# Kernel optimization log

Hardware: AMD Instinct MI355X
Metric: run time of the kernel (lower is better)

## Reference

```python
import jax, jax.numpy as jnp
import numpy as np
from jax import lax

T, N, E, F, H, L, HL = 16, 10000, 320000, 128, 256, 64, 256


def setup_inputs() -> dict:
    key = jax.random.key(0)
    ks = iter(jax.random.split(key, 40))
    def nrm(shape, fan_in):
        return jax.random.normal(next(ks), shape, jnp.float32) * (1.0 / np.sqrt(fan_in))
    inp = {}
    inp["xs"] = jax.random.normal(next(ks), (T, N, F), jnp.float32)
    inp["edge_attr"] = jax.random.uniform(next(ks), (E,), jnp.float32)
    # encoder: GCN(F->H), GCN(H->H), Linear(H->L)
    inp["We0"], inp["be0"] = nrm((F, H), F), nrm((H,), H)
    inp["We1"], inp["be1"] = nrm((H, H), H), nrm((H,), H)
    inp["Wfce"], inp["bfce"] = nrm((H, L), H), nrm((L,), L)
    # 2-layer LSTM (torch gate order i,f,g,o; weights stored [in,4H])
    inp["Wih0"], inp["Whh0"] = nrm((L, 4 * HL), HL), nrm((HL, 4 * HL), HL)
    inp["bih0"], inp["bhh0"] = nrm((4 * HL,), HL), nrm((4 * HL,), HL)
    inp["Wih1"], inp["Whh1"] = nrm((HL, 4 * HL), HL), nrm((HL, 4 * HL), HL)
    inp["bih1"], inp["bhh1"] = nrm((4 * HL,), HL), nrm((4 * HL,), HL)
    inp["Whead"], inp["bhead"] = nrm((HL, L), HL), nrm((L,), L)
    # decoder: Linear(L -> N*L), GCN(L->H), GCN(H->H), GCN(H->F)
    inp["Wfcd"], inp["bfcd"] = nrm((L, N * L), L), nrm((N * L,), L)
    inp["Wd0"], inp["bd0"] = nrm((L, H), L), nrm((H,), H)
    inp["Wd1"], inp["bd1"] = nrm((H, H), H), nrm((H,), H)
    inp["Wd2"], inp["bd2"] = nrm((H, F), H), nrm((F,), F)
    inp["edge_index"] = jax.random.randint(next(ks), (2, E), 0, N, jnp.int64)
    return inp


def _forward(xs, edge_attr, We0, be0, We1, be1, Wfce, bfce,
             Wih0, Whh0, bih0, bhh0, Wih1, Whh1, bih1, bhh1,
             Whead, bhead, Wfcd, bfcd, Wd0, bd0, Wd1, bd1, Wd2, bd2,
             edge_index):
    n = xs.shape[1]
    loops = jnp.arange(n)
    src = jnp.concatenate([edge_index[0], loops])  # [E+N] with self-loops
    dst = jnp.concatenate([edge_index[1], loops])

    def gcn(x, ew, W, b):
        # PyG GCNConv: x@W then D^-1/2 A D^-1/2 scatter-add, + bias
        deg = jax.ops.segment_sum(ew, dst, num_segments=n)
        dis = jnp.where(deg > 0, lax.rsqrt(deg), 0.0)
        norm = dis[src] * ew * dis[dst]          # [E+N]
        h = x @ W                                # [N, Fout]
        return jax.ops.segment_sum(norm[:, None] * h[src], dst, num_segments=n) + b

    ew_enc = jnp.concatenate([edge_attr, jnp.ones((n,), edge_attr.dtype)])
    ew_dec = jnp.ones((src.shape[0],), xs.dtype)

    def encode(x):
        x = jax.nn.relu(gcn(x, ew_enc, We0, be0))
        x = jax.nn.relu(gcn(x, ew_enc, We1, be1))
        g = x.mean(axis=0)                       # global_mean_pool (single graph)
        return g @ Wfce + bfce                   # [L]

    zs = jax.vmap(encode)(xs)                    # [T, L]

    def lstm_layer(seq, Wih, Whh, bih, bhh):
        hdim = Whh.shape[0]
        def step(carry, xt):
            h, c = carry
            g = xt @ Wih + h @ Whh + bih + bhh
            i, f, gg, o = jnp.split(g, 4)
            c = jax.nn.sigmoid(f) * c + jax.nn.sigmoid(i) * jnp.tanh(gg)
            h = jax.nn.sigmoid(o) * jnp.tanh(c)
            return (h, c), h
        init = (jnp.zeros((hdim,), seq.dtype), jnp.zeros((hdim,), seq.dtype))
        return lax.scan(step, init, seq)[1]

    h1 = lstm_layer(zs, Wih0, Whh0, bih0, bhh0)
    h2 = lstm_layer(h1, Wih1, Whh1, bih1, bhh1)
    z = (h2 @ Whead + bhead)[-1]                 # last timestep, [L]

    x = jax.nn.relu(z @ Wfcd + bfcd).reshape(n, -1)  # [N, L]
    x = jax.nn.relu(gcn(x, ew_dec, Wd0, bd0))
    x = jax.nn.relu(gcn(x, ew_dec, Wd1, bd1))
    return gcn(x, ew_dec, Wd2, bd2)              # [N, F]


def reference(xs, edge_attr, We0, be0, We1, be1, Wfce, bfce,
              Wih0, Whh0, bih0, bhh0, Wih1, Whh1, bih1, bhh1,
              Whead, bhead, Wfcd, bfcd, Wd0, bd0, Wd1, bd1, Wd2, bd2,
              edge_index):
    return _forward(xs, edge_attr, We0, be0, We1, be1, Wfce, bfce,
                    Wih0, Whh0, bih0, bhh0, Wih1, Whh1, bih1, bhh1,
                    Whead, bhead, Wfcd, bfcd, Wd0, bd0, Wd1, bd1, Wd2, bd2,
                    edge_index)
```

## Files before the change

kernel.cpp:

```cpp
#include <hip/hip_runtime.h>
#include <math.h>

#define TT 16
#define NN 10000
#define EE 320000
#define FF 128
#define HH 256
#define LL 64
#define HLL 256

typedef _Float16 h16;
typedef _Float16 half4 __attribute__((ext_vector_type(4)));
typedef _Float16 half8 __attribute__((ext_vector_type(8)));
typedef float floatx4 __attribute__((ext_vector_type(4)));

__device__ __forceinline__ float sigm(float x) { return 1.0f / (1.0f + expf(-x)); }


__global__ void pre_deg(const int* __restrict__ src, const int* __restrict__ dst,
                        const float* __restrict__ ea, float* __restrict__ deg_enc,
                        int* __restrict__ cnt) {
    int e = blockIdx.x * 256 + threadIdx.x;
    if (e >= EE) return;
    int d = dst[e];
    atomicAdd(&deg_enc[d], ea[e]);
    atomicAdd(&cnt[d], 1);
}

__global__ void pre_dis(const float* __restrict__ deg_enc, const int* __restrict__ cnt,
                        float* __restrict__ dis_enc, float* __restrict__ dis_dec,
                        float* __restrict__ sn_enc, float* __restrict__ sn_dec) {
    int n = blockIdx.x * 256 + threadIdx.x;
    if (n >= NN) return;
    float de = deg_enc[n] + 1.0f;
    float dd = (float)cnt[n] + 1.0f;
    dis_enc[n] = rsqrtf(de);
    dis_dec[n] = rsqrtf(dd);
    sn_enc[n] = 1.0f / de;
    sn_dec[n] = 1.0f / dd;
}

__global__ void scan_rowptr(const int* __restrict__ cnt, int* __restrict__ row_ptr) {
    __shared__ int sb[1024];
    int tx = threadIdx.x;
    int run = 0;
    if (tx == 0) row_ptr[0] = 0;
    for (int base = 0; base < NN; base += 1024) {
        int i = base + tx;
        int v = (i < NN) ? cnt[i] : 0;
        sb[tx] = v;
        __syncthreads();
        for (int off = 1; off < 1024; off <<= 1) {
            int t = (tx >= off) ? sb[tx - off] : 0;
            __syncthreads();
            sb[tx] += t;
            __syncthreads();
        }
        if (i < NN) row_ptr[i + 1] = run + sb[tx];
        run += sb[1023];
        __syncthreads();
    }
}

__global__ void pre_build(const int* __restrict__ src, const int* __restrict__ dst,
                          const float* __restrict__ ea, const int* __restrict__ row_ptr,
                          int* __restrict__ cursor, const float* __restrict__ dis_enc,
                          const float* __restrict__ dis_dec, int* __restrict__ src_s,
                          float* __restrict__ w_enc, float* __restrict__ w_dec) {
    int e = blockIdx.x * 256 + threadIdx.x;
    if (e >= EE) return;
    int s = src[e], d = dst[e];
    int pos = row_ptr[d] + atomicAdd(&cursor[d], 1);
    src_s[pos] = s;
    w_enc[pos] = dis_enc[s] * ea[e] * dis_enc[d];
    w_dec[pos] = dis_dec[s] * dis_dec[d];
}


__global__ void cvt_f2h(const float* __restrict__ src, h16* __restrict__ dst, long n4) {
    long i = (long)blockIdx.x * 256 + threadIdx.x;
    if (i >= n4) return;
    float4 v = ((const float4*)src)[i];
    half4 o = {(h16)v.x, (h16)v.y, (h16)v.z, (h16)v.w};
    ((half4*)dst)[i] = o;
}

__global__ void wcvt(const float* __restrict__ Wsrc, h16* __restrict__ WT, int K, int N) {
    int i = blockIdx.x * 256 + threadIdx.x;
    if (i >= K * N) return;
    int n = i / K, k = i % K;
    WT[i] = (h16)Wsrc[(long)k * N + n];
}

template <int LPE, bool BIAS, bool RELU, bool OUT32>
__global__ __launch_bounds__(256) void spmm2(
    const h16* __restrict__ in, void* __restrict__ outv,
    const int* __restrict__ rp, const int* __restrict__ srcs,
    const float* __restrict__ w, const float* __restrict__ selfw,
    const float* __restrict__ bias, long sIn, long sOut) {
    constexpr int EPW = 64 / LPE;
    const half8* in8 = (const half8*)(in + (long)blockIdx.z * sIn);
    int wv = threadIdx.x >> 6;
    int node = blockIdx.x * 4 + wv;
    int lane = threadIdx.x & 63;
    int c8 = lane & (LPE - 1);
    int el = lane / LPE;
    float acc[8] = {0.f, 0.f, 0.f, 0.f, 0.f, 0.f, 0.f, 0.f};
    if (el == 0) {
        half8 sv = in8[(long)node * LPE + c8];
        float sw = selfw[node];
#pragma unroll
        for (int i = 0; i < 8; ++i) acc[i] = sw * (float)sv[i];
    }
    int r1 = rp[node + 1];
    int j = rp[node] + el;
    for (; j + EPW < r1; j += 2 * EPW) {
        int sA = srcs[j], sB = srcs[j + EPW];
        float wA = w[j], wB = w[j + EPW];
        half8 vA = in8[(long)sA * LPE + c8];
        half8 vB = in8[(long)sB * LPE + c8];
#pragma unroll
        for (int i = 0; i < 8; ++i) acc[i] += wA * (float)vA[i] + wB * (float)vB[i];
    }
    if (j < r1) {
        float wA = w[j];
        half8 vA = in8[(long)srcs[j] * LPE + c8];
#pragma unroll
        for (int i = 0; i < 8; ++i) acc[i] += wA * (float)vA[i];
    }
#pragma unroll
    for (int m = LPE; m < 64; m <<= 1) {
#pragma unroll
        for (int i = 0; i < 8; ++i) acc[i] += __shfl_xor(acc[i], m);
    }
    if (el == 0) {
        if (BIAS) {
            float4 b0 = *(const float4*)&bias[c8 * 8];
            float4 b1 = *(const float4*)&bias[c8 * 8 + 4];
            acc[0] += b0.x; acc[1] += b0.y; acc[2] += b0.z; acc[3] += b0.w;
            acc[4] += b1.x; acc[5] += b1.y; acc[6] += b1.z; acc[7] += b1.w;
        }
        if (RELU) {
#pragma unroll
            for (int i = 0; i < 8; ++i) acc[i] = fmaxf(acc[i], 0.f);
        }
        if (OUT32) {
            float* o = (float*)outv + (long)blockIdx.z * sOut + (long)node * (LPE * 8) + c8 * 8;
            *(float4*)o = make_float4(acc[0], acc[1], acc[2], acc[3]);
            *(float4*)(o + 4) = make_float4(acc[4], acc[5], acc[6], acc[7]);
        } else {
            half8 ov = {(h16)acc[0], (h16)acc[1], (h16)acc[2], (h16)acc[3],
                        (h16)acc[4], (h16)acc[5], (h16)acc[6], (h16)acc[7]};
            ((half8*)((h16*)outv + (long)blockIdx.z * sOut))[(long)node * LPE + c8] = ov;
        }
    }
}

template <bool BIAS, bool RELU>
__global__ __launch_bounds__(256) void gemm_h(
    const h16* __restrict__ A, const h16* __restrict__ BT,
    const float* __restrict__ bias, h16* __restrict__ C,
    int M, int Nc, int K, long sA, long sC) {
    A += (long)blockIdx.z * sA;
    C += (long)blockIdx.z * sC;
    __shared__ h16 smem[5120];
    h16* As = smem;
    h16* Bs = smem + 2560;
    int tid = threadIdx.x;
    int bm = blockIdx.y * 64, bn = blockIdx.x * 64;
    int w = tid >> 6, lane = tid & 63;
    int l15 = lane & 15, quad = lane >> 4;
    int srow = tid >> 2, skseg = (tid & 3) * 8;
    floatx4 acc[4] = {{0, 0, 0, 0}, {0, 0, 0, 0}, {0, 0, 0, 0}, {0, 0, 0, 0}};
    for (int k0 = 0; k0 < K; k0 += 32) {
        half8 av = {};
        if (bm + srow < M) av = *(const half8*)&A[(long)(bm + srow) * K + k0 + skseg];
        *(half8*)&As[srow * 40 + skseg] = av;
        *(half8*)&Bs[srow * 40 + skseg] = *(const half8*)&BT[(long)(bn + srow) * K + k0 + skseg];
        __syncthreads();
        half8 af = *(const half8*)&As[(w * 16 + l15) * 40 + quad * 8];
#pragma unroll
        for (int nt = 0; nt < 4; ++nt) {
            half8 bf = *(const half8*)&Bs[(nt * 16 + l15) * 40 + quad * 8];
            acc[nt] = __builtin_amdgcn_mfma_f32_16x16x32_f16(af, bf, acc[nt], 0, 0, 0);
        }
        __syncthreads();
    }
    h16* Cs = smem;
#pragma unroll
    for (int nt = 0; nt < 4; ++nt) {
        int col = bn + nt * 16 + l15;
        float b = BIAS ? bias[col] : 0.0f;
#pragma unroll
        for (int r = 0; r < 4; ++r) {
            float v = acc[nt][r] + b;
            if (RELU) v = fmaxf(v, 0.0f);
            Cs[(w * 16 + quad * 4 + r) * 72 + nt * 16 + l15] = (h16)v;
        }
    }
    __syncthreads();
    int orow = tid >> 2, oseg = (tid & 3) * 16;
    if (bm + orow < M) {
        half8 v0 = *(const half8*)&Cs[orow * 72 + oseg];
        half8 v1 = *(const half8*)&Cs[orow * 72 + oseg + 8];
        *(half8*)&C[(long)(bm + orow) * Nc + bn + oseg] = v0;
        *(half8*)&C[(long)(bm + orow) * Nc + bn + oseg + 8] = v1;
    }
}

__global__ void col_mean_h(const h16* __restrict__ in, float* __restrict__ pooled, long sIn) {
    const h16* p = in + (long)blockIdx.z * sIn;
    float* pt = pooled + (long)blockIdx.z * HH;
    int c = threadIdx.x;
    int n0 = blockIdx.x * 64;
    int n1 = min(n0 + 64, NN);
    float acc = 0.f;
    for (int n = n0; n < n1; ++n) acc += (float)p[(long)n * HH + c];
    atomicAdd(&pt[c], acc * (1.0f / (float)NN));
}

__global__ void enc_head(const float* __restrict__ pooled, const float* __restrict__ Wfce,
                         const float* __restrict__ bfce, float* __restrict__ z) {
    int t = blockIdx.x, j = threadIdx.x;
    __shared__ float p[HH];
    for (int i = j; i < HH; i += 64) p[i] = pooled[t * HH + i];
    __syncthreads();
    float acc = bfce[j];
    for (int h = 0; h < HH; ++h) acc += p[h] * Wfce[h * LL + j];
    z[t * LL + j] = acc;
}

__global__ __launch_bounds__(256) void fused_lstm(
    const float* __restrict__ zenc,
    const float* __restrict__ Wih0, const float* __restrict__ Whh0,
    const float* __restrict__ bih0, const float* __restrict__ bhh0,
    const float* __restrict__ Wih1, const float* __restrict__ Whh1,
    const float* __restrict__ bih1, const float* __restrict__ bhh1,
    const float* __restrict__ Whead, const float* __restrict__ bhead,
    float* __restrict__ H1, float* __restrict__ H2,
    unsigned* __restrict__ bar, float* __restrict__ zdec) {
    __shared__ h16 Ws[256][64];
    __shared__ float Gs[16][64];
    __shared__ float part[4][64];
    __shared__ float hbuf[256];
    __shared__ float cbuf[16];
    int tid = threadIdx.x;
    int kq = tid >> 6;
    int col = tid & 63;
    int g4 = col >> 4, ul = col & 15;
    int u0 = blockIdx.x * 16;
    int jg = g4 * 256 + u0 + ul;
    unsigned gen = 0;

#define GBAR()                                                        \
    do {                                                              \
        __threadfence();                                              \
        __syncthreads();                                              \
        if (tid == 0) {                                               \
            ++gen;                                                    \
            atomicAdd(bar, 1u);                                       \
            while (atomicAdd(bar, 0u) < 16u * gen)                    \
                __builtin_amdgcn_s_sleep(2);                          \
        }                                                             \
        __syncthreads();                                              \
        __threadfence();                                              \
    } while (0)

    if (tid < 16) cbuf[tid] = 0.f;
    for (int idx = tid; idx < 256 * 64; idx += 256) {
        int k = idx >> 6, c = idx & 63;
        Ws[k][c] = (h16)Whh0[k * 1024 + (c >> 4) * 256 + u0 + (c & 15)];
    }
    {
        float b = bih0[jg] + bhh0[jg];
        float a0 = b, a1 = b, a2 = b, a3 = b;
        for (int k = 0; k < 64; ++k) {
            float wvv = Wih0[k * 1024 + jg];
            a0 += zenc[kq * 64 + k] * wvv;
            a1 += zenc[(kq + 4) * 64 + k] * wvv;
            a2 += zenc[(kq + 8) * 64 + k] * wvv;
            a3 += zenc[(kq + 12) * 64 + k] * wvv;
        }
        Gs[kq][col] = a0; Gs[kq + 4][col] = a1;
        Gs[kq + 8][col] = a2; Gs[kq + 12][col] = a3;
    }
    __syncthreads();
    for (int t = 1; t <= 16; ++t) {
        hbuf[tid] = H1[(t - 1) * 256 + tid];
        __syncthreads();
        float acc = 0.f;
#pragma unroll
        for (int i = 0; i < 64; ++i) acc += hbuf[kq * 64 + i] * (float)Ws[kq * 64 + i][col];
        part[kq][col] = acc;
        __syncthreads();
        if (tid < 16) {
            int u = tid;
            float i_ = Gs[t - 1][u]      + part[0][u]      + part[1][u]      + part[2][u]      + part[3][u];
            float f_ = Gs[t - 1][16 + u] + part[0][16 + u] + part[1][16 + u] + part[2][16 + u] + part[3][16 + u];
            float g_ = Gs[t - 1][32 + u] + part[0][32 + u] + part[1][32 + u] + part[2][32 + u] + part[3][32 + u];
            float o_ = Gs[t - 1][48 + u] + part[0][48 + u] + part[1][48 + u] + part[2][48 + u] + part[3][48 + u];
            float cc = sigm(f_) * cbuf[u] + sigm(i_) * tanhf(g_);
            cbuf[u] = cc;
            H1[t * 256 + u0 + u] = sigm(o_) * tanhf(cc);
        }
        GBAR();
    }
    if (tid < 16) cbuf[tid] = 0.f;
    for (int idx = tid; idx < 256 * 64; idx += 256) {
        int k = idx >> 6, c = idx & 63;
        Ws[k][c] = (h16)Whh1[k * 1024 + (c >> 4) * 256 + u0 + (c & 15)];
    }
    {
        float b = bih1[jg] + bhh1[jg];
        float a0 = b, a1 = b, a2 = b, a3 = b;
        for (int k = 0; k < 256; ++k) {
            float wvv = Wih1[k * 1024 + jg];
            a0 += H1[(kq + 1) * 256 + k] * wvv;
            a1 += H1[(kq + 5) * 256 + k] * wvv;
            a2 += H1[(kq + 9) * 256 + k] * wvv;
            a3 += H1[(kq + 13) * 256 + k] * wvv;
        }
        Gs[kq][col] = a0; Gs[kq + 4][col] = a1;
        Gs[kq + 8][col] = a2; Gs[kq + 12][col] = a3;
    }
    __syncthreads();
    for (int t = 1; t <= 16; ++t) {
        hbuf[tid] = H2[(t - 1) * 256 + tid];
        __syncthreads();
        float acc = 0.f;
#pragma unroll
        for (int i = 0; i < 64; ++i) acc += hbuf[kq * 64 + i] * (float)Ws[kq * 64 + i][col];
        part[kq][col] = acc;
        __syncthreads();
        if (tid < 16) {
            int u = tid;
            float i_ = Gs[t - 1][u]      + part[0][u]      + part[1][u]      + part[2][u]      + part[3][u];
            float f_ = Gs[t - 1][16 + u] + part[0][16 + u] + part[1][16 + u] + part[2][16 + u] + part[3][16 + u];
            float g_ = Gs[t - 1][32 + u] + part[0][32 + u] + part[1][32 + u] + part[2][32 + u] + part[3][32 + u];
            float o_ = Gs[t - 1][48 + u] + part[0][48 + u] + part[1][48 + u] + part[2][48 + u] + part[3][48 + u];
            float cc = sigm(f_) * cbuf[u] + sigm(i_) * tanhf(g_);
            cbuf[u] = cc;
            H2[t * 256 + u0 + u] = sigm(o_) * tanhf(cc);
        }
        GBAR();
    }
    if (blockIdx.x == 0 && tid < 64) {
        const float* hf = H2 + 16 * 256;
        float a = bhead[tid];
        for (int k = 0; k < 256; ++k) a += hf[k] * Whead[k * 64 + tid];
        zdec[tid] = a;
    }
#undef GBAR
}

__global__ void dec_fc(const float* __restrict__ z, const float* __restrict__ Wfcd,
                       const float* __restrict__ bfcd, h16* __restrict__ Xd) {
    __shared__ float zs_[LL];
    if (threadIdx.x < LL) zs_[threadIdx.x] = z[threadIdx.x];
    __syncthreads();
    long m = ((long)blockIdx.x * 256 + threadIdx.x) * 4;
    if (m >= (long)NN * LL) return;
    float4 acc = *(const float4*)&bfcd[m];
#pragma unroll
    for (int k = 0; k < LL; ++k) {
        float4 w4 = *(const float4*)&Wfcd[(long)k * (NN * (long)LL) + m];
        float zk = zs_[k];
        acc.x += zk * w4.x; acc.y += zk * w4.y; acc.z += zk * w4.z; acc.w += zk * w4.w;
    }
    half4 o = {(h16)fmaxf(acc.x, 0.f), (h16)fmaxf(acc.y, 0.f),
               (h16)fmaxf(acc.z, 0.f), (h16)fmaxf(acc.w, 0.f)};
    *(half4*)&Xd[m] = o;
}


extern "C" void kernel_launch(void* const* d_in, const int* in_sizes, int n_in,
                              void* d_out, int out_size, void* d_ws, size_t ws_size,
                              hipStream_t stream) {
    const float* xs = (const float*)d_in[0];
    const float* edge_attr = (const float*)d_in[1];
    const float* We0 = (const float*)d_in[2];  const float* be0 = (const float*)d_in[3];
    const float* We1 = (const float*)d_in[4];  const float* be1 = (const float*)d_in[5];
    const float* Wfce = (const float*)d_in[6]; const float* bfce = (const float*)d_in[7];
    const float* Wih0 = (const float*)d_in[8]; const float* Whh0 = (const float*)d_in[9];
    const float* bih0 = (const float*)d_in[10]; const float* bhh0 = (const float*)d_in[11];
    const float* Wih1 = (const float*)d_in[12]; const float* Whh1 = (const float*)d_in[13];
    const float* bih1 = (const float*)d_in[14]; const float* bhh1 = (const float*)d_in[15];
    const float* Whead = (const float*)d_in[16]; const float* bhead = (const float*)d_in[17];
    const float* Wfcd = (const float*)d_in[18]; const float* bfcd = (const float*)d_in[19];
    const float* Wd0 = (const float*)d_in[20]; const float* bd0 = (const float*)d_in[21];
    const float* Wd1 = (const float*)d_in[22]; const float* bd1 = (const float*)d_in[23];
    const float* Wd2 = (const float*)d_in[24]; const float* bd2 = (const float*)d_in[25];
    const int* eidx = (const int*)d_in[26];
    const int* esrc = eidx;
    const int* edst = eidx + EE;
    float* out = (float*)d_out;
    float* W = (float*)d_ws;

    const long O_DEG = 0;
    const long O_CNT = 10000;
    const long O_CUR = 20000;
    const long O_POOL = 30000;
    const long O_H1 = 34096;
    const long O_H2 = 38448;
    const long O_BAR = 42800;
    const long ZFLOATS = 42816;
    const long O_DISE = 42816, O_DISD = 52816, O_SNE = 62816, O_SND = 72816;
    const long O_RP = 82816;
    const long O_SRCS = 92832;
    const long O_WENC = 412832;
    const long O_WDEC = 732832;
    const long O_ZENC = 1052832;
    const long O_ZDEC = 1053856;
    const long O_F16 = 1053920;

    h16* Hbase = (h16*)(W + O_F16);
    const long HO_XS = 0;
    const long HO_WE0T = 20480000;
    const long HO_WE1T = HO_WE0T + 32768;
    const long HO_WD0T = HO_WE1T + 65536;
    const long HO_WD1T = HO_WD0T + 16384;
    const long HO_WD2T = HO_WD1T + 65536;
    const long HO_XD = HO_WD2T + 32768;
    const long HO_B0 = HO_XD + 640000;

    const long SB0 = (long)NN * FF;
    const long SB1 = (long)NN * HH;

    const long needBatched = O_F16 * 4 + (HO_B0 + 16L * (SB0 + 2 * SB1)) * 2;
    const bool batched = (long)ws_size >= needBatched;
    const long tb = batched ? 16 : 1;
    const long hoB1 = HO_B0 + tb * SB0;
    const long hoB2 = hoB1 + tb * SB1;

    float* deg = W + O_DEG;
    int* cnt = (int*)(W + O_CNT);
    int* cur = (int*)(W + O_CUR);
    float* pooled = W + O_POOL;
    float* H1 = W + O_H1; float* H2 = W + O_H2;
    unsigned* bar = (unsigned*)(W + O_BAR);
    float* dise = W + O_DISE; float* disd = W + O_DISD;
    float* sne = W + O_SNE;   float* snd = W + O_SND;
    int* rp = (int*)(W + O_RP);
    int* srcs = (int*)(W + O_SRCS);
    float* wenc = W + O_WENC; float* wdec = W + O_WDEC;
    float* zenc = W + O_ZENC; float* zdec = W + O_ZDEC;
    h16* xsh = Hbase + HO_XS;
    h16* We0T = Hbase + HO_WE0T; h16* We1T = Hbase + HO_WE1T;
    h16* Wd0T = Hbase + HO_WD0T; h16* Wd1T = Hbase + HO_WD1T; h16* Wd2T = Hbase + HO_WD2T;
    h16* XDh = Hbase + HO_XD;
    h16* B0h = Hbase + HO_B0; h16* B1h = Hbase + hoB1; h16* B2h = Hbase + hoB2;

    hipMemsetAsync(d_ws, 0, ZFLOATS * 4, stream);
    pre_deg<<<(EE + 255) / 256, 256, 0, stream>>>(esrc, edst, edge_attr, deg, cnt);
    pre_dis<<<(NN + 255) / 256, 256, 0, stream>>>(deg, cnt, dise, disd, sne, snd);
    scan_rowptr<<<1, 1024, 0, stream>>>(cnt, rp);
    pre_build<<<(EE + 255) / 256, 256, 0, stream>>>(esrc, edst, edge_attr, rp, cur, dise, disd,
                                                    srcs, wenc, wdec);
    cvt_f2h<<<20000, 256, 0, stream>>>(xs, xsh, (long)TT * NN * FF / 4);
    wcvt<<<(FF * HH + 255) / 256, 256, 0, stream>>>(We0, We0T, FF, HH);
    wcvt<<<(HH * HH + 255) / 256, 256, 0, stream>>>(We1, We1T, HH, HH);
    wcvt<<<(LL * HH + 255) / 256, 256, 0, stream>>>(Wd0, Wd0T, LL, HH);
    wcvt<<<(HH * HH + 255) / 256, 256, 0, stream>>>(Wd1, Wd1T, HH, HH);
    wcvt<<<(HH * FF + 255) / 256, 256, 0, stream>>>(Wd2, Wd2T, HH, FF);

    if (batched) {
        spmm2<16, false, false, false><<<dim3(2500, 1, 16), 256, 0, stream>>>(
            xsh, B0h, rp, srcs, wenc, sne, nullptr, SB0, SB0);
        gemm_h<true, true><<<dim3(4, 157, 16), 256, 0, stream>>>(
            B0h, We0T, be0, B1h, NN, HH, FF, SB0, SB1);
        gemm_h<false, false><<<dim3(4, 157, 16), 256, 0, stream>>>(
            B1h, We1T, nullptr, B2h, NN, HH, HH, SB1, SB1);
        spmm2<32, true, true, false><<<dim3(2500, 1, 16), 256, 0, stream>>>(
            B2h, B1h, rp, srcs, wenc, sne, be1, SB1, SB1);
        col_mean_h<<<dim3(157, 1, 16), 256, 0, stream>>>(B1h, pooled, SB1);
    } else {
        for (int t = 0; t < TT; ++t) {
            spmm2<16, false, false, false><<<dim3(2500, 1, 1), 256, 0, stream>>>(
                xsh + (long)t * SB0, B0h, rp, srcs, wenc, sne, nullptr, 0, 0);
            gemm_h<true, true><<<dim3(4, 157, 1), 256, 0, stream>>>(
                B0h, We0T, be0, B1h, NN, HH, FF, 0, 0);
            gemm_h<false, false><<<dim3(4, 157, 1), 256, 0, stream>>>(
                B1h, We1T, nullptr, B2h, NN, HH, HH, 0, 0);
            spmm2<32, true, true, false><<<dim3(2500, 1, 1), 256, 0, stream>>>(
                B2h, B1h, rp, srcs, wenc, sne, be1, 0, 0);
            col_mean_h<<<dim3(157, 1, 1), 256, 0, stream>>>(B1h, pooled + t * HH, 0);
        }
    }
    enc_head<<<16, 64, 0, stream>>>(pooled, Wfce, bfce, zenc);

    fused_lstm<<<16, 256, 0, stream>>>(zenc, Wih0, Whh0, bih0, bhh0,
                                       Wih1, Whh1, bih1, bhh1,
                                       Whead, bhead, H1, H2, bar, zdec);

    dec_fc<<<625, 256, 0, stream>>>(zdec, Wfcd, bfcd, XDh);
    spmm2<8, false, false, false><<<dim3(2500, 1, 1), 256, 0, stream>>>(
        XDh, B0h, rp, srcs, wdec, snd, nullptr, 0, 0);
    gemm_h<true, true><<<dim3(4, 157, 1), 256, 0, stream>>>(
        B0h, Wd0T, bd0, B1h, NN, HH, LL, 0, 0);
    gemm_h<false, false><<<dim3(4, 157, 1), 256, 0, stream>>>(
        B1h, Wd1T, nullptr, B2h, NN, HH, HH, 0, 0);
    spmm2<32, true, true, false><<<dim3(2500, 1, 1), 256, 0, stream>>>(
        B2h, B1h, rp, srcs, wdec, snd, bd1, 0, 0);
    gemm_h<false, false><<<dim3(2, 157, 1), 256, 0, stream>>>(
        B1h, Wd2T, nullptr, B0h, NN, FF, HH, 0, 0);
    spmm2<16, true, false, true><<<dim3(2500, 1, 1), 256, 0, stream>>>(
        B0h, out, rp, srcs, wdec, snd, bd2, 0, 0);
}
```

Measured before the change: 1.151 ms.

## Interleave SpMM timesteps per block, unroll gather 4x, widen GEMM tile to 128 rows

The SpMM grid is flattened so that groups of 8 consecutive blocks handle the same node block across 8 timesteps. Blocks that share the same neighbor indices and weights then run close together, which should improve L2 reuse of the CSR data. The edge gather loop is unrolled from 2 to 4 to keep more loads in flight. The GEMM tile grows from 64 to 128 rows per block, with two MFMA row-fragments per wave, so B-tile loads are reused more and fewer blocks are launched. The cost is higher register and LDS use per block.

```diff
diff --git a/kernel.cpp b/kernel.cpp
--- a/kernel.cpp
+++ b/kernel.cpp
@@ -97,11 +97,22 @@
     const h16* __restrict__ in, void* __restrict__ outv,
     const int* __restrict__ rp, const int* __restrict__ srcs,
     const float* __restrict__ w, const float* __restrict__ selfw,
-    const float* __restrict__ bias, long sIn, long sOut) {
+    const float* __restrict__ bias, long sIn, long sOut, int tbatch) {
     constexpr int EPW = 64 / LPE;
-    const half8* in8 = (const half8*)(in + (long)blockIdx.z * sIn);
+    int g = blockIdx.x;
+    int z, nb;
+    if (tbatch > 1) {
+        int gz = g & 7;
+        int ph = g >> 3;
+        nb = ph % (NN / 4);
+        z = (ph / (NN / 4)) * 8 + gz;
+    } else {
+        z = 0;
+        nb = g;
+    }
+    const half8* in8 = (const half8*)(in + (long)z * sIn);
     int wv = threadIdx.x >> 6;
-    int node = blockIdx.x * 4 + wv;
+    int node = nb * 4 + wv;
     int lane = threadIdx.x & 63;
     int c8 = lane & (LPE - 1);
     int el = lane / LPE;
@@ -114,15 +125,18 @@
     }
     int r1 = rp[node + 1];
     int j = rp[node] + el;
-    for (; j + EPW < r1; j += 2 * EPW) {
-        int sA = srcs[j], sB = srcs[j + EPW];
-        float wA = w[j], wB = w[j + EPW];
-        half8 vA = in8[(long)sA * LPE + c8];
-        half8 vB = in8[(long)sB * LPE + c8];
-#pragma unroll
-        for (int i = 0; i < 8; ++i) acc[i] += wA * (float)vA[i] + wB * (float)vB[i];
-    }
-    if (j < r1) {
+    for (; j + 3 * EPW < r1; j += 4 * EPW) {
+        int s0 = srcs[j], s1 = srcs[j + EPW], s2 = srcs[j + 2 * EPW], s3 = srcs[j + 3 * EPW];
+        float w0 = w[j], w1 = w[j + EPW], w2 = w[j + 2 * EPW], w3 = w[j + 3 * EPW];
+        half8 v0 = in8[(long)s0 * LPE + c8];
+        half8 v1 = in8[(long)s1 * LPE + c8];
+        half8 v2 = in8[(long)s2 * LPE + c8];
+        half8 v3 = in8[(long)s3 * LPE + c8];
+#pragma unroll
+        for (int i = 0; i < 8; ++i)
+            acc[i] += w0 * (float)v0[i] + w1 * (float)v1[i] + w2 * (float)v2[i] + w3 * (float)v3[i];
+    }
+    for (; j < r1; j += EPW) {
         float wA = w[j];
         half8 vA = in8[(long)srcs[j] * LPE + c8];
 #pragma unroll
@@ -145,13 +159,13 @@
             for (int i = 0; i < 8; ++i) acc[i] = fmaxf(acc[i], 0.f);
         }
         if (OUT32) {
-            float* o = (float*)outv + (long)blockIdx.z * sOut + (long)node * (LPE * 8) + c8 * 8;
+            float* o = (float*)outv + (long)z * sOut + (long)node * (LPE * 8) + c8 * 8;
             *(float4*)o = make_float4(acc[0], acc[1], acc[2], acc[3]);
             *(float4*)(o + 4) = make_float4(acc[4], acc[5], acc[6], acc[7]);
         } else {
             half8 ov = {(h16)acc[0], (h16)acc[1], (h16)acc[2], (h16)acc[3],
                         (h16)acc[4], (h16)acc[5], (h16)acc[6], (h16)acc[7]};
-            ((half8*)((h16*)outv + (long)blockIdx.z * sOut))[(long)node * LPE + c8] = ov;
+            ((half8*)((h16*)outv + (long)z * sOut))[(long)node * LPE + c8] = ov;
         }
     }
 }
@@ -163,48 +177,57 @@
     int M, int Nc, int K, long sA, long sC) {
     A += (long)blockIdx.z * sA;
     C += (long)blockIdx.z * sC;
-    __shared__ h16 smem[5120];
+    __shared__ h16 smem[9216];
     h16* As = smem;
-    h16* Bs = smem + 2560;
+    h16* Bs = smem + 5120;
     int tid = threadIdx.x;
-    int bm = blockIdx.y * 64, bn = blockIdx.x * 64;
+    int bm = blockIdx.y * 128, bn = blockIdx.x * 64;
     int w = tid >> 6, lane = tid & 63;
     int l15 = lane & 15, quad = lane >> 4;
-    int srow = tid >> 2, skseg = (tid & 3) * 8;
-    floatx4 acc[4] = {{0, 0, 0, 0}, {0, 0, 0, 0}, {0, 0, 0, 0}, {0, 0, 0, 0}};
+    int ar = tid >> 2, ks = (tid & 3) * 8;
+    floatx4 acc[2][4] = {};
     for (int k0 = 0; k0 < K; k0 += 32) {
-        half8 av = {};
-        if (bm + srow < M) av = *(const half8*)&A[(long)(bm + srow) * K + k0 + skseg];
-        *(half8*)&As[srow * 40 + skseg] = av;
-        *(half8*)&Bs[srow * 40 + skseg] = *(const half8*)&BT[(long)(bn + srow) * K + k0 + skseg];
-        __syncthreads();
-        half8 af = *(const half8*)&As[(w * 16 + l15) * 40 + quad * 8];
+        half8 a0 = {}, a1 = {};
+        if (bm + ar < M) a0 = *(const half8*)&A[(long)(bm + ar) * K + k0 + ks];
+        if (bm + ar + 64 < M) a1 = *(const half8*)&A[(long)(bm + ar + 64) * K + k0 + ks];
+        *(half8*)&As[ar * 40 + ks] = a0;
+        *(half8*)&As[(ar + 64) * 40 + ks] = a1;
+        *(half8*)&Bs[ar * 40 + ks] = *(const half8*)&BT[(long)(bn + ar) * K + k0 + ks];
+        __syncthreads();
+        half8 af0 = *(const half8*)&As[(w * 32 + l15) * 40 + quad * 8];
+        half8 af1 = *(const half8*)&As[(w * 32 + 16 + l15) * 40 + quad * 8];
 #pragma unroll
         for (int nt = 0; nt < 4; ++nt) {
             half8 bf = *(const half8*)&Bs[(nt * 16 + l15) * 40 + quad * 8];
-            acc[nt] = __builtin_amdgcn_mfma_f32_16x16x32_f16(af, bf, acc[nt], 0, 0, 0);
+            acc[0][nt] = __builtin_amdgcn_mfma_f32_16x16x32_f16(af0, bf, acc[0][nt], 0, 0, 0);
+            acc[1][nt] = __builtin_amdgcn_mfma_f32_16x16x32_f16(af1, bf, acc[1][nt], 0, 0, 0);
         }
         __syncthreads();
     }
     h16* Cs = smem;
 #pragma unroll
     for (int nt = 0; nt < 4; ++nt) {
-        int col = bn + nt * 16 + l15;
-        float b = BIAS ? bias[col] : 0.0f;
-#pragma unroll
-        for (int r = 0; r < 4; ++r) {
-            float v = acc[nt][r] + b;
-            if (RELU) v = fmaxf(v, 0.0f);
-            Cs[(w * 16 + quad * 4 + r) * 72 + nt * 16 + l15] = (h16)v;
+        float b = BIAS ? bias[bn + nt * 16 + l15] : 0.0f;
+#pragma unroll
+        for (int mf = 0; mf < 2; ++mf) {
+#pragma unroll
+            for (int r = 0; r < 4; ++r) {
+                float v = acc[mf][nt][r] + b;
+                if (RELU) v = fmaxf(v, 0.0f);
+                Cs[(w * 32 + mf * 16 + quad * 4 + r) * 72 + nt * 16 + l15] = (h16)v;
+            }
         }
     }
     __syncthreads();
-    int orow = tid >> 2, oseg = (tid & 3) * 16;
-    if (bm + orow < M) {
-        half8 v0 = *(const half8*)&Cs[orow * 72 + oseg];
-        half8 v1 = *(const half8*)&Cs[orow * 72 + oseg + 8];
-        *(half8*)&C[(long)(bm + orow) * Nc + bn + oseg] = v0;
-        *(half8*)&C[(long)(bm + orow) * Nc + bn + oseg + 8] = v1;
+#pragma unroll
+    for (int p = 0; p < 2; ++p) {
+        int r = (tid >> 2) + p * 64, sg = (tid & 3) * 16;
+        if (bm + r < M) {
+            half8 v0 = *(const half8*)&Cs[r * 72 + sg];
+            half8 v1 = *(const half8*)&Cs[r * 72 + sg + 8];
+            *(half8*)&C[(long)(bm + r) * Nc + bn + sg] = v0;
+            *(half8*)&C[(long)(bm + r) * Nc + bn + sg + 8] = v1;
+        }
     }
 }
 
@@ -464,25 +487,25 @@
     wcvt<<<(HH * FF + 255) / 256, 256, 0, stream>>>(Wd2, Wd2T, HH, FF);
 
     if (batched) {
-        spmm2<16, false, false, false><<<dim3(2500, 1, 16), 256, 0, stream>>>(
-            xsh, B0h, rp, srcs, wenc, sne, nullptr, SB0, SB0);
-        gemm_h<true, true><<<dim3(4, 157, 16), 256, 0, stream>>>(
+        spmm2<16, false, false, false><<<dim3(2500 * 16), 256, 0, stream>>>(
+            xsh, B0h, rp, srcs, wenc, sne, nullptr, SB0, SB0, 16);
+        gemm_h<true, true><<<dim3(4, 79, 16), 256, 0, stream>>>(
             B0h, We0T, be0, B1h, NN, HH, FF, SB0, SB1);
-        gemm_h<false, false><<<dim3(4, 157, 16), 256, 0, stream>>>(
+        gemm_h<false, false><<<dim3(4, 79, 16), 256, 0, stream>>>(
             B1h, We1T, nullptr, B2h, NN, HH, HH, SB1, SB1);
-        spmm2<32, true, true, false><<<dim3(2500, 1, 16), 256, 0, stream>>>(
-            B2h, B1h, rp, srcs, wenc, sne, be1, SB1, SB1);
+        spmm2<32, true, true, false><<<dim3(2500 * 16), 256, 0, stream>>>(
+            B2h, B1h, rp, srcs, wenc, sne, be1, SB1, SB1, 16);
         col_mean_h<<<dim3(157, 1, 16), 256, 0, stream>>>(B1h, pooled, SB1);
     } else {
         for (int t = 0; t < TT; ++t) {
-            spmm2<16, false, false, false><<<dim3(2500, 1, 1), 256, 0, stream>>>(
-                xsh + (long)t * SB0, B0h, rp, srcs, wenc, sne, nullptr, 0, 0);
-            gemm_h<true, true><<<dim3(4, 157, 1), 256, 0, stream>>>(
+            spmm2<16, false, false, false><<<dim3(2500), 256, 0, stream>>>(
+                xsh + (long)t * SB0, B0h, rp, srcs, wenc, sne, nullptr, 0, 0, 1);
+            gemm_h<true, true><<<dim3(4, 79, 1), 256, 0, stream>>>(
                 B0h, We0T, be0, B1h, NN, HH, FF, 0, 0);
-            gemm_h<false, false><<<dim3(4, 157, 1), 256, 0, stream>>>(
+            gemm_h<false, false><<<dim3(4, 79, 1), 256, 0, stream>>>(
                 B1h, We1T, nullptr, B2h, NN, HH, HH, 0, 0);
-            spmm2<32, true, true, false><<<dim3(2500, 1, 1), 256, 0, stream>>>(
-                B2h, B1h, rp, srcs, wenc, sne, be1, 0, 0);
+            spmm2<32, true, true, false><<<dim3(2500), 256, 0, stream>>>(
+                B2h, B1h, rp, srcs, wenc, sne, be1, 0, 0, 1);
             col_mean_h<<<dim3(157, 1, 1), 256, 0, stream>>>(B1h, pooled + t * HH, 0);
         }
     }
@@ -493,16 +516,16 @@
                                        Whead, bhead, H1, H2, bar, zdec);
 
     dec_fc<<<625, 256, 0, stream>>>(zdec, Wfcd, bfcd, XDh);
-    spmm2<8, false, false, false><<<dim3(2500, 1, 1), 256, 0, stream>>>(
-        XDh, B0h, rp, srcs, wdec, snd, nullptr, 0, 0);
-    gemm_h<true, true><<<dim3(4, 157, 1), 256, 0, stream>>>(
+    spmm2<8, false, false, false><<<dim3(2500), 256, 0, stream>>>(
+        XDh, B0h, rp, srcs, wdec, snd, nullptr, 0, 0, 1);
+    gemm_h<true, true><<<dim3(4, 79, 1), 256, 0, stream>>>(
         B0h, Wd0T, bd0, B1h, NN, HH, LL, 0, 0);
-    gemm_h<false, false><<<dim3(4, 157, 1), 256, 0, stream>>>(
+    gemm_h<false, false><<<dim3(4, 79, 1), 256, 0, stream>>>(
         B1h, Wd1T, nullptr, B2h, NN, HH, HH, 0, 0);
-    spmm2<32, true, true, false><<<dim3(2500, 1, 1), 256, 0, stream>>>(
-        B2h, B1h, rp, srcs, wdec, snd, bd1, 0, 0);
-    gemm_h<false, false><<<dim3(2, 157, 1), 256, 0, stream>>>(
+    spmm2<32, true, true, false><<<dim3(2500), 256, 0, stream>>>(
+        B2h, B1h, rp, srcs, wdec, snd, bd1, 0, 0, 1);
+    gemm_h<false, false><<<dim3(2, 79, 1), 256, 0, stream>>>(
         B1h, Wd2T, nullptr, B0h, NN, FF, HH, 0, 0);
-    spmm2<16, true, false, true><<<dim3(2500, 1, 1), 256, 0, stream>>>(
-        B0h, out, rp, srcs, wdec, snd, bd2, 0, 0);
-}
+    spmm2<16, true, false, true><<<dim3(2500), 256, 0, stream>>>(
+        B0h, out, rp, srcs, wdec, snd, bd2, 0, 0, 1);
+}
```

Measured after the change: 1.094 ms. 1.05x faster.
